# Kernel tuning notes

Hardware: AMD Instinct MI355X
Metric: run time of the kernel (lower is better)

The kernel has to match this reference:

```python
import jax, jax.numpy as jnp
import numpy as np

B, P, E, H = 2, 4096, 512, 8
D = E // H
EPS = 1e-5


def _layernorm2d(x, g, b):
    # LayerNorm over last two dims (patches, embed) jointly, per torch nn.LayerNorm([P, E])
    mu = jnp.mean(x, axis=(-2, -1), keepdims=True)
    var = jnp.mean(jnp.square(x - mu), axis=(-2, -1), keepdims=True)
    return (x - mu) * jax.lax.rsqrt(var + EPS) * g + b


def setup_inputs() -> dict:
    key = jax.random.key(0)
    ks = jax.random.split(key, 4)
    s_in = 1.0 / np.sqrt(E)
    s_hid = 1.0 / np.sqrt(3 * E)
    return {
        "x": jax.random.normal(ks[0], (B, P, E), dtype=jnp.float32),
        "g1": jnp.ones((P, E), jnp.float32),
        "b1": jnp.zeros((P, E), jnp.float32),
        "W1": jax.random.normal(ks[1], (3 * E, E), jnp.float32) * s_in,
        "g2": jnp.ones((P, E), jnp.float32),
        "b2": jnp.zeros((P, E), jnp.float32),
        "Wa": jax.random.normal(ks[2], (3 * E, E), jnp.float32) * s_in,
        "ba": jnp.zeros((3 * E,), jnp.float32),
        "Wb": jax.random.normal(ks[3], (E, 3 * E), jnp.float32) * s_hid,
        "bb": jnp.zeros((E,), jnp.float32),
    }


def reference(x, g1, b1, W1, g2, b2, Wa, ba, Wb, bb):
    # --- attention branch ---
    h = _layernorm2d(x, g1, b1)                      # [B,P,E]
    qkv = h @ W1.T                                   # [B,P,3E]
    qkv = qkv.reshape(B, P, 3, H, D).transpose(2, 0, 3, 1, 4)  # [3,B,H,P,D]
    q, k, v = qkv[0], qkv[1], qkv[2]
    scale = 1.0 / jnp.sqrt(jnp.float32(D))
    dp = jnp.einsum("bhqd,bhkd->bhqk", q, k) * scale  # [B,H,P,P]
    # NOTE: softmax over axis -2 (the query axis), as in the original code
    dp = jax.nn.softmax(dp, axis=-2)
    wv = jnp.einsum("bhqk,bhkd->bhqd", dp, v)        # [B,H,P,D]
    wv = wv.transpose(0, 2, 1, 3).reshape(B, P, E)   # [B,P,E]
    out1 = x + wv
    # --- MLP branch ---
    h2 = _layernorm2d(out1, g2, b2)
    h2 = jax.nn.gelu(h2 @ Wa.T + ba, approximate=False)
    h2 = jax.nn.gelu(h2 @ Wb.T + bb, approximate=False)
    return h2 + out1
```

## Files before the change

### kernel.cpp

```cpp
#include <hip/hip_runtime.h>
#include <math.h>

typedef __bf16 bf16x8 __attribute__((ext_vector_type(8)));
typedef float f32x4 __attribute__((ext_vector_type(4)));
typedef unsigned short u16;
typedef unsigned int u32;

__device__ __forceinline__ void gl_lds16(const void* g, void* l) {
  __builtin_amdgcn_global_load_lds(
      (const __attribute__((address_space(1))) void*)g,
      (__attribute__((address_space(3))) void*)l, 16, 0, 0);
}

__device__ __forceinline__ u16 f2bf(float x) {
  union { float f; u32 u; } v; v.f = x;
  u32 r = v.u + 0x7FFFu + ((v.u >> 16) & 1u);
  return (u16)(r >> 16);
}

__device__ __forceinline__ float gelu_f(float v) {
  return 0.5f * v * (1.0f + erff(v * 0.7071067811865475f));
}

__global__ void castbf(const float* __restrict__ s, u16* __restrict__ d) {
  int i = blockIdx.x * 256 + threadIdx.x;
  float4 v = ((const float4*)s)[i];
  uint2 o;
  o.x = (u32)f2bf(v.x) | ((u32)f2bf(v.y) << 16);
  o.y = (u32)f2bf(v.z) | ((u32)f2bf(v.w) << 16);
  ((uint2*)d)[i] = o;
}

__global__ void ln_reduce(const float* __restrict__ src, float2* __restrict__ part) {
  int b = blockIdx.y;
  const float4* p = (const float4*)(src + (size_t)b * 2097152 + (size_t)blockIdx.x * 16384);
  float s = 0.f, q = 0.f;
  #pragma unroll
  for (int i = 0; i < 16; i++) {
    float4 v = p[i * 256 + threadIdx.x];
    s += v.x + v.y + v.z + v.w;
    q += v.x * v.x + v.y * v.y + v.z * v.z + v.w * v.w;
  }
  #pragma unroll
  for (int off = 32; off; off >>= 1) { s += __shfl_down(s, off, 64); q += __shfl_down(q, off, 64); }
  __shared__ float ls[4], lq[4];
  int w = threadIdx.x >> 6;
  if ((threadIdx.x & 63) == 0) { ls[w] = s; lq[w] = q; }
  __syncthreads();
  if (threadIdx.x == 0)
    part[b * 128 + blockIdx.x] =
        make_float2(ls[0] + ls[1] + ls[2] + ls[3], lq[0] + lq[1] + lq[2] + lq[3]);
}

__global__ void ln_final(const float2* __restrict__ part, float2* __restrict__ stats) {
  int b = blockIdx.x, t = threadIdx.x;
  float2 a = part[b * 128 + t], c = part[b * 128 + 64 + t];
  float s = a.x + c.x, q = a.y + c.y;
  #pragma unroll
  for (int off = 32; off; off >>= 1) { s += __shfl_down(s, off, 64); q += __shfl_down(q, off, 64); }
  if (t == 0) {
    const float inv = 1.0f / 2097152.0f;
    float mu = s * inv, var = q * inv - mu * mu;
    stats[b] = make_float2(mu, rsqrtf(var + 1e-5f));
  }
}

__global__ void ln_apply(const float* __restrict__ src, const float* __restrict__ g,
                         const float* __restrict__ bta, const float2* __restrict__ stats,
                         u16* __restrict__ dst) {
  int i = blockIdx.x * 256 + threadIdx.x;
  int b = i >= 524288;
  float2 st = stats[b];
  int r = i - b * 524288;
  float4 v = ((const float4*)src)[i];
  float4 gv = ((const float4*)g)[r];
  float4 bv = ((const float4*)bta)[r];
  float h0 = (v.x - st.x) * st.y * gv.x + bv.x;
  float h1 = (v.y - st.x) * st.y * gv.y + bv.y;
  float h2 = (v.z - st.x) * st.y * gv.z + bv.z;
  float h3 = (v.w - st.x) * st.y * gv.w + bv.w;
  uint2 o;
  o.x = (u32)f2bf(h0) | ((u32)f2bf(h1) << 16);
  o.y = (u32)f2bf(h2) | ((u32)f2bf(h3) << 16);
  ((uint2*)dst)[i] = o;
}

template <int MODE>
__global__ __launch_bounds__(256, 2)
void gemm_bt(const u16* __restrict__ A, const u16* __restrict__ Bm,
             const float* __restrict__ bias, const float* __restrict__ res,
             float* __restrict__ outf, u16* __restrict__ outb,
             int M, int N, int K) {
  __shared__ u16 As[128 * 32], Bs[128 * 32];
  const int tid = threadIdx.x;
  const int m0 = blockIdx.y * 128, n0 = blockIdx.x * 128;
  const int lane = tid & 63, w = tid >> 6;
  const int wm = (w >> 1) * 64, wn = (w & 1) * 64;
  const int c = lane & 15, quad = lane >> 4;
  const int arow = tid >> 2, acol = (tid & 3) * 8;

  const u16* gA = A + (size_t)(m0 + arow) * K + acol;
  const u16* gB = Bm + (size_t)(n0 + arow) * K + acol;
  u16* lA = As + tid * 8;
  u16* lB = Bs + tid * 8;

  f32x4 acc[4][4] = {};
  for (int kt = 0; kt < K; kt += 32) {
    gl_lds16(gA, lA);
    gl_lds16(gA + (size_t)64 * K, lA + 64 * 32);
    gl_lds16(gB, lB);
    gl_lds16(gB + (size_t)64 * K, lB + 64 * 32);
    gA += 32; gB += 32;
    __syncthreads();
    bf16x8 af[4], bf[4];
    #pragma unroll
    for (int i = 0; i < 4; i++) {
      af[i] = *(const bf16x8*)&As[(wm + i * 16 + c) * 32 + quad * 8];
      bf[i] = *(const bf16x8*)&Bs[(wn + i * 16 + c) * 32 + quad * 8];
    }
    #pragma unroll
    for (int i = 0; i < 4; i++)
      #pragma unroll
      for (int j = 0; j < 4; j++)
        acc[i][j] = __builtin_amdgcn_mfma_f32_16x16x32_bf16(af[i], bf[j], acc[i][j], 0, 0, 0);
    __syncthreads();
  }
  #pragma unroll
  for (int i = 0; i < 4; i++) {
    const int row0 = m0 + wm + i * 16 + quad * 4;
    #pragma unroll
    for (int j = 0; j < 4; j++) {
      const int col = n0 + wn + j * 16 + c;
      #pragma unroll
      for (int r = 0; r < 4; r++) {
        float v = acc[i][j][r];
        size_t oi = (size_t)(row0 + r) * N + col;
        if (MODE == 1 || MODE == 2) v = gelu_f(v + bias[col]);
        if (MODE == 2) outf[oi] = v + res[oi];
        else           outb[oi] = f2bf(v);
      }
    }
  }
}

__global__ void vtrans(const u16* __restrict__ qkv, u16* __restrict__ vt) {
  __shared__ u16 t[64 * 66];
  int bh = blockIdx.y, p0 = blockIdx.x * 64;
  int b = bh >> 3, h = bh & 7;
  const u16* src = qkv + ((size_t)(b * 4096 + p0)) * 1536 + 1024 + h * 64;
  int tid = threadIdx.x;
  #pragma unroll
  for (int j = 0; j < 16; j++) {
    int idx = j * 256 + tid;
    int p = idx >> 6, d = idx & 63;
    t[d * 66 + p] = src[(size_t)p * 1536 + d];
  }
  __syncthreads();
  u16* dst = vt + (size_t)bh * 64 * 4096 + p0;
  #pragma unroll
  for (int j = 0; j < 16; j++) {
    int idx = j * 256 + tid;
    int d = idx >> 6, p = idx & 63;
    dst[(size_t)d * 4096 + p] = t[d * 66 + p];
  }
}

__global__ __launch_bounds__(256, 2)
void attn_pass1(const u16* __restrict__ qkv, float* __restrict__ rl) {
  __shared__ u16 Ks[2 * 128 * 32], Qs[2 * 128 * 32];
  __shared__ float colsum[128];
  const int tid = threadIdx.x;
  const int bh = blockIdx.y, b = bh >> 3, h = bh & 7;
  const int k0 = blockIdx.x * 128;
  const int lane = tid & 63, w = tid >> 6;
  const int wm = (w >> 1) * 64, wn = (w & 1) * 64;
  const int c = lane & 15, quad = lane >> 4;
  const int arow = tid >> 2, acol = (tid & 3) * 8;
  const u16* Kg = qkv + ((size_t)(b * 4096 + k0)) * 1536 + 512 + h * 64;
  const u16* Qg = qkv + ((size_t)(b * 4096)) * 1536 + h * 64;

  #pragma unroll
  for (int ks = 0; ks < 2; ks++)
    #pragma unroll
    for (int rr = 0; rr < 128; rr += 64)
      gl_lds16(Kg + (size_t)(rr + arow) * 1536 + ks * 32 + acol,
               Ks + ks * 4096 + (rr + arow) * 32 + acol);
  if (tid < 128) colsum[tid] = 0.f;

  float sacc[4] = {0.f, 0.f, 0.f, 0.f};
  for (int qt = 0; qt < 32; qt++) {
    #pragma unroll
    for (int ks = 0; ks < 2; ks++)
      #pragma unroll
      for (int rr = 0; rr < 128; rr += 64)
        gl_lds16(Qg + (size_t)(qt * 128 + rr + arow) * 1536 + ks * 32 + acol,
                 Qs + ks * 4096 + (rr + arow) * 32 + acol);
    __syncthreads();
    f32x4 acc[4][4] = {};
    #pragma unroll
    for (int ks = 0; ks < 2; ks++) {
      bf16x8 af[4], bf[4];
      #pragma unroll
      for (int i = 0; i < 4; i++) {
        af[i] = *(const bf16x8*)&Qs[ks * 4096 + (wm + i * 16 + c) * 32 + quad * 8];
        bf[i] = *(const bf16x8*)&Ks[ks * 4096 + (wn + i * 16 + c) * 32 + quad * 8];
      }
      #pragma unroll
      for (int i = 0; i < 4; i++)
        #pragma unroll
        for (int j = 0; j < 4; j++)
          acc[i][j] = __builtin_amdgcn_mfma_f32_16x16x32_bf16(af[i], bf[j], acc[i][j], 0, 0, 0);
    }
    #pragma unroll
    for (int j = 0; j < 4; j++) {
      float t = 0.f;
      #pragma unroll
      for (int i = 0; i < 4; i++)
        #pragma unroll
        for (int r = 0; r < 4; r++)
          t += __expf(acc[i][j][r] * 0.125f);
      sacc[j] += t;
    }
    __syncthreads();
  }
  #pragma unroll
  for (int j = 0; j < 4; j++) {
    float v = sacc[j];
    v += __shfl_xor(v, 16, 64);
    v += __shfl_xor(v, 32, 64);
    if (quad == 0) atomicAdd(&colsum[wn + j * 16 + c], v);
  }
  __syncthreads();
  if (tid < 128) rl[(size_t)bh * 4096 + k0 + tid] = 1.0f / colsum[tid];
}

__global__ __launch_bounds__(256, 2)
void attn_pass2(const u16* __restrict__ qkv, const u16* __restrict__ vt,
                const float* __restrict__ rl, const float* __restrict__ x,
                float* __restrict__ out1) {
  __shared__ u16 Qs[2 * 128 * 32];
  __shared__ u16 Ks[2 * 128 * 32];
  __shared__ u16 Vs[4 * 64 * 32];
  __shared__ u16 Ps[4 * 128 * 32];
  const int tid = threadIdx.x;
  const int bh = blockIdx.y, b = bh >> 3, h = bh & 7;
  const int q0 = blockIdx.x * 128;
  const int lane = tid & 63, w = tid >> 6;
  const int wm = (w >> 1) * 64, wn = (w & 1) * 64;
  const int wn2 = (w & 1) * 32;
  const int c = lane & 15, quad = lane >> 4;
  const int arow = tid >> 2, acol = (tid & 3) * 8;
  const u16* Qg = qkv + ((size_t)(b * 4096 + q0)) * 1536 + h * 64;
  const u16* Kg = qkv + ((size_t)(b * 4096)) * 1536 + 512 + h * 64;
  const u16* Vg = vt + (size_t)bh * 64 * 4096;
  const float* rlg = rl + (size_t)bh * 4096;

  #pragma unroll
  for (int ks = 0; ks < 2; ks++)
    #pragma unroll
    for (int rr = 0; rr < 128; rr += 64)
      gl_lds16(Qg + (size_t)(rr + arow) * 1536 + ks * 32 + acol,
               Qs + ks * 4096 + (rr + arow) * 32 + acol);

  f32x4 oacc[4][2] = {};
  for (int kt = 0; kt < 32; kt++) {
    const int k0 = kt * 128;
    #pragma unroll
    for (int ks = 0; ks < 2; ks++)
      #pragma unroll
      for (int rr = 0; rr < 128; rr += 64)
        gl_lds16(Kg + (size_t)(k0 + rr + arow) * 1536 + ks * 32 + acol,
                 Ks + ks * 4096 + (rr + arow) * 32 + acol);
    #pragma unroll
    for (int kp = 0; kp < 4; kp++)
      gl_lds16(Vg + (size_t)arow * 4096 + k0 + kp * 32 + acol,
               Vs + kp * 2048 + arow * 32 + acol);
    __syncthreads();
    f32x4 sacc[4][4] = {};
    #pragma unroll
    for (int ks = 0; ks < 2; ks++) {
      bf16x8 af[4], bf[4];
      #pragma unroll
      for (int i = 0; i < 4; i++) {
        af[i] = *(const bf16x8*)&Qs[ks * 4096 + (wm + i * 16 + c) * 32 + quad * 8];
        bf[i] = *(const bf16x8*)&Ks[ks * 4096 + (wn + i * 16 + c) * 32 + quad * 8];
      }
      #pragma unroll
      for (int i = 0; i < 4; i++)
        #pragma unroll
        for (int j = 0; j < 4; j++)
          sacc[i][j] = __builtin_amdgcn_mfma_f32_16x16x32_bf16(af[i], bf[j], sacc[i][j], 0, 0, 0);
    }
    float rlv[4];
    #pragma unroll
    for (int j = 0; j < 4; j++) rlv[j] = rlg[k0 + wn + j * 16 + c];
    #pragma unroll
    for (int i = 0; i < 4; i++)
      #pragma unroll
      for (int j = 0; j < 4; j++) {
        const int kk = wn + j * 16 + c;
        u16* pp = Ps + (kk >> 5) * 4096 + (kk & 31);
        #pragma unroll
        for (int r = 0; r < 4; r++) {
          const int qq = wm + i * 16 + quad * 4 + r;
          pp[qq * 32] = f2bf(__expf(sacc[i][j][r] * 0.125f) * rlv[j]);
        }
      }
    __syncthreads();
    #pragma unroll
    for (int ks = 0; ks < 4; ks++) {
      bf16x8 pf[4], vf[2];
      #pragma unroll
      for (int i = 0; i < 4; i++)
        pf[i] = *(const bf16x8*)&Ps[ks * 4096 + (wm + i * 16 + c) * 32 + quad * 8];
      #pragma unroll
      for (int j = 0; j < 2; j++)
        vf[j] = *(const bf16x8*)&Vs[ks * 2048 + (wn2 + j * 16 + c) * 32 + quad * 8];
      #pragma unroll
      for (int i = 0; i < 4; i++)
        #pragma unroll
        for (int j = 0; j < 2; j++)
          oacc[i][j] = __builtin_amdgcn_mfma_f32_16x16x32_bf16(pf[i], vf[j], oacc[i][j], 0, 0, 0);
    }
    __syncthreads();
  }
  #pragma unroll
  for (int i = 0; i < 4; i++)
    #pragma unroll
    for (int j = 0; j < 2; j++)
      #pragma unroll
      for (int r = 0; r < 4; r++) {
        const int qq = q0 + wm + i * 16 + quad * 4 + r;
        const int dd = wn2 + j * 16 + c;
        size_t oi = ((size_t)(b * 4096 + qq)) * 512 + h * 64 + dd;
        out1[oi] = x[oi] + oacc[i][j][r];
      }
}

extern "C" void kernel_launch(void* const* d_in, const int* in_sizes, int n_in,
                              void* d_out, int out_size, void* d_ws, size_t ws_size,
                              hipStream_t stream) {
  const float* x  = (const float*)d_in[0];
  const float* g1 = (const float*)d_in[1];
  const float* b1 = (const float*)d_in[2];
  const float* W1 = (const float*)d_in[3];
  const float* g2 = (const float*)d_in[4];
  const float* b2 = (const float*)d_in[5];
  const float* Wa = (const float*)d_in[6];
  const float* ba = (const float*)d_in[7];
  const float* Wb = (const float*)d_in[8];
  const float* bb = (const float*)d_in[9];
  float* out = (float*)d_out;

  char* ws = (char*)d_ws;
  u16* w1b   = (u16*)(ws);
  u16* wab   = (u16*)(ws + 1572864);
  u16* wbb   = (u16*)(ws + 3145728);
  u16* h1    = (u16*)(ws + 4718592);
  u16* qkv   = (u16*)(ws + 13107200);
  u16* vt    = (u16*)(ws + 38273024);
  u16* h2    = (u16*)(ws + 46661632);
  u16* mid   = (u16*)(ws + 55050240);
  float* rl  = (float*)(ws + 80216064);
  float* o1  = (float*)(ws + 80478208);
  float2* part  = (float2*)(ws + 97255424);
  float2* stats = (float2*)(ws + 97257472);

  castbf<<<768, 256, 0, stream>>>(W1, w1b);
  castbf<<<768, 256, 0, stream>>>(Wa, wab);
  castbf<<<768, 256, 0, stream>>>(Wb, wbb);

  ln_reduce<<<dim3(128, 2), 256, 0, stream>>>(x, part);
  ln_final<<<2, 64, 0, stream>>>(part, stats);
  ln_apply<<<4096, 256, 0, stream>>>(x, g1, b1, stats, h1);

  gemm_bt<0><<<dim3(12, 64), 256, 0, stream>>>(h1, w1b, nullptr, nullptr, nullptr, qkv,
                                               8192, 1536, 512);
  vtrans<<<dim3(64, 16), 256, 0, stream>>>(qkv, vt);
  attn_pass1<<<dim3(32, 16), 256, 0, stream>>>(qkv, rl);
  attn_pass2<<<dim3(32, 16), 256, 0, stream>>>(qkv, vt, rl, x, o1);

  ln_reduce<<<dim3(128, 2), 256, 0, stream>>>(o1, part);
  ln_final<<<2, 64, 0, stream>>>(part, stats);
  ln_apply<<<4096, 256, 0, stream>>>(o1, g2, b2, stats, h2);

  gemm_bt<1><<<dim3(12, 64), 256, 0, stream>>>(h2, wab, ba, nullptr, nullptr, mid,
                                               8192, 1536, 512);
  gemm_bt<2><<<dim3(4, 64), 256, 0, stream>>>(mid, wbb, bb, o1, out, nullptr,
                                              8192, 512, 1536);
}
```

Before: 417.7 us.

## Fold column-softmax normalization into V and restructure attention passes around register-held Q/K

Pre-scales Q by 1/sqrt(D) in the QKV GEMM epilogue and folds the per-key reciprocal column sum into V during the transpose, so pass2 no longer reads rl or multiplies per element. Pass1 is rewritten to keep each wave's K fragments in registers and stream Q straight from global memory, with no LDS or block syncs. Pass2 keeps Q fragments in registers, computes transposed score tiles, writes packed bf16 P into a swizzled LDS layout, and drops one barrier per iteration. The three weight casts are merged into one launch. Costs include an extra rounding of V and Q to bf16 and global-latency exposure in pass1.

Result: slower. 454.1 us (+8.7%).

```diff
diff --git a/kernel.cpp b/kernel.cpp
--- a/kernel.cpp
+++ b/kernel.cpp
@@ -18,12 +18,24 @@
   return (u16)(r >> 16);
 }
 
+__device__ __forceinline__ u32 pack_bf2(float a, float b) {
+  union { float f; u32 u; } ua, ub; ua.f = a; ub.f = b;
+  return ((ua.u + 0x8000u) >> 16) | ((ub.u + 0x8000u) & 0xFFFF0000u);
+}
+
 __device__ __forceinline__ float gelu_f(float v) {
   return 0.5f * v * (1.0f + erff(v * 0.7071067811865475f));
 }
 
-__global__ void castbf(const float* __restrict__ s, u16* __restrict__ d) {
-  int i = blockIdx.x * 256 + threadIdx.x;
+__global__ void castbf3(const float* __restrict__ s0, const float* __restrict__ s1,
+                        const float* __restrict__ s2, u16* __restrict__ d0,
+                        u16* __restrict__ d1, u16* __restrict__ d2) {
+  int blk = blockIdx.x;
+  const float* s; u16* d;
+  if (blk < 768)       { s = s0; d = d0; }
+  else if (blk < 1536) { s = s1; d = d1; blk -= 768; }
+  else                 { s = s2; d = d2; blk -= 1536; }
+  int i = blk * 256 + threadIdx.x;
   float4 v = ((const float4*)s)[i];
   uint2 o;
   o.x = (u32)f2bf(v.x) | ((u32)f2bf(v.y) << 16);
@@ -135,6 +147,7 @@
       for (int r = 0; r < 4; r++) {
         float v = acc[i][j][r];
         size_t oi = (size_t)(row0 + r) * N + col;
+        if (MODE == 0 && col < 512) v *= 0.125f;
         if (MODE == 1 || MODE == 2) v = gelu_f(v + bias[col]);
         if (MODE == 2) outf[oi] = v + res[oi];
         else           outb[oi] = f2bf(v);
@@ -143,17 +156,71 @@
   }
 }
 
-__global__ void vtrans(const u16* __restrict__ qkv, u16* __restrict__ vt) {
+__global__ __launch_bounds__(256, 2)
+void attn_pass1(const u16* __restrict__ qkv, float* __restrict__ rl) {
+  const int tid = threadIdx.x;
+  const int bh = blockIdx.y, b = bh >> 3, h = bh & 7;
+  const int k0 = blockIdx.x * 128;
+  const int lane = tid & 63, w = tid >> 6;
+  const int wn = w * 32;
+  const int c = lane & 15, quad = lane >> 4;
+
+  bf16x8 bk[2][2];
+  {
+    const u16* Kg = qkv + ((size_t)(b * 4096 + k0 + wn + c)) * 1536 + 512 + h * 64 + quad * 8;
+    #pragma unroll
+    for (int j = 0; j < 2; j++)
+      #pragma unroll
+      for (int ks = 0; ks < 2; ks++)
+        bk[j][ks] = *(const bf16x8*)(Kg + (size_t)j * 16 * 1536 + ks * 32);
+  }
+  const u16* Qg = qkv + ((size_t)(b * 4096 + c)) * 1536 + h * 64 + quad * 8;
+
+  float s0 = 0.f, s1 = 0.f;
+  for (int qt = 0; qt < 64; qt++) {
+    f32x4 acc[4][2] = {};
+    #pragma unroll
+    for (int i4 = 0; i4 < 4; i4++) {
+      const u16* qp = Qg + (size_t)(qt * 64 + i4 * 16) * 1536;
+      bf16x8 a0 = *(const bf16x8*)(qp);
+      bf16x8 a1 = *(const bf16x8*)(qp + 32);
+      acc[i4][0] = __builtin_amdgcn_mfma_f32_16x16x32_bf16(a0, bk[0][0], acc[i4][0], 0, 0, 0);
+      acc[i4][0] = __builtin_amdgcn_mfma_f32_16x16x32_bf16(a1, bk[0][1], acc[i4][0], 0, 0, 0);
+      acc[i4][1] = __builtin_amdgcn_mfma_f32_16x16x32_bf16(a0, bk[1][0], acc[i4][1], 0, 0, 0);
+      acc[i4][1] = __builtin_amdgcn_mfma_f32_16x16x32_bf16(a1, bk[1][1], acc[i4][1], 0, 0, 0);
+    }
+    #pragma unroll
+    for (int i4 = 0; i4 < 4; i4++) {
+      #pragma unroll
+      for (int r = 0; r < 4; r++) {
+        s0 += __expf(acc[i4][0][r]);
+        s1 += __expf(acc[i4][1][r]);
+      }
+    }
+  }
+  s0 += __shfl_xor(s0, 16, 64); s0 += __shfl_xor(s0, 32, 64);
+  s1 += __shfl_xor(s1, 16, 64); s1 += __shfl_xor(s1, 32, 64);
+  if (quad == 0) {
+    rl[(size_t)bh * 4096 + k0 + wn + c]      = 1.0f / s0;
+    rl[(size_t)bh * 4096 + k0 + wn + 16 + c] = 1.0f / s1;
+  }
+}
+
+__global__ void vtrans(const u16* __restrict__ qkv, const float* __restrict__ rl,
+                       u16* __restrict__ vt) {
   __shared__ u16 t[64 * 66];
   int bh = blockIdx.y, p0 = blockIdx.x * 64;
   int b = bh >> 3, h = bh & 7;
   const u16* src = qkv + ((size_t)(b * 4096 + p0)) * 1536 + 1024 + h * 64;
+  const float* rp = rl + (size_t)bh * 4096 + p0;
   int tid = threadIdx.x;
   #pragma unroll
   for (int j = 0; j < 16; j++) {
     int idx = j * 256 + tid;
     int p = idx >> 6, d = idx & 63;
-    t[d * 66 + p] = src[(size_t)p * 1536 + d];
+    union { float f; u32 u; } uv;
+    uv.u = ((u32)src[(size_t)p * 1536 + d]) << 16;
+    t[d * 66 + p] = f2bf(uv.f * rp[p]);
   }
   __syncthreads();
   u16* dst = vt + (size_t)bh * 64 * 4096 + p0;
@@ -166,79 +233,8 @@
 }
 
 __global__ __launch_bounds__(256, 2)
-void attn_pass1(const u16* __restrict__ qkv, float* __restrict__ rl) {
-  __shared__ u16 Ks[2 * 128 * 32], Qs[2 * 128 * 32];
-  __shared__ float colsum[128];
-  const int tid = threadIdx.x;
-  const int bh = blockIdx.y, b = bh >> 3, h = bh & 7;
-  const int k0 = blockIdx.x * 128;
-  const int lane = tid & 63, w = tid >> 6;
-  const int wm = (w >> 1) * 64, wn = (w & 1) * 64;
-  const int c = lane & 15, quad = lane >> 4;
-  const int arow = tid >> 2, acol = (tid & 3) * 8;
-  const u16* Kg = qkv + ((size_t)(b * 4096 + k0)) * 1536 + 512 + h * 64;
-  const u16* Qg = qkv + ((size_t)(b * 4096)) * 1536 + h * 64;
-
-  #pragma unroll
-  for (int ks = 0; ks < 2; ks++)
-    #pragma unroll
-    for (int rr = 0; rr < 128; rr += 64)
-      gl_lds16(Kg + (size_t)(rr + arow) * 1536 + ks * 32 + acol,
-               Ks + ks * 4096 + (rr + arow) * 32 + acol);
-  if (tid < 128) colsum[tid] = 0.f;
-
-  float sacc[4] = {0.f, 0.f, 0.f, 0.f};
-  for (int qt = 0; qt < 32; qt++) {
-    #pragma unroll
-    for (int ks = 0; ks < 2; ks++)
-      #pragma unroll
-      for (int rr = 0; rr < 128; rr += 64)
-        gl_lds16(Qg + (size_t)(qt * 128 + rr + arow) * 1536 + ks * 32 + acol,
-                 Qs + ks * 4096 + (rr + arow) * 32 + acol);
-    __syncthreads();
-    f32x4 acc[4][4] = {};
-    #pragma unroll
-    for (int ks = 0; ks < 2; ks++) {
-      bf16x8 af[4], bf[4];
-      #pragma unroll
-      for (int i = 0; i < 4; i++) {
-        af[i] = *(const bf16x8*)&Qs[ks * 4096 + (wm + i * 16 + c) * 32 + quad * 8];
-        bf[i] = *(const bf16x8*)&Ks[ks * 4096 + (wn + i * 16 + c) * 32 + quad * 8];
-      }
-      #pragma unroll
-      for (int i = 0; i < 4; i++)
-        #pragma unroll
-        for (int j = 0; j < 4; j++)
-          acc[i][j] = __builtin_amdgcn_mfma_f32_16x16x32_bf16(af[i], bf[j], acc[i][j], 0, 0, 0);
-    }
-    #pragma unroll
-    for (int j = 0; j < 4; j++) {
-      float t = 0.f;
-      #pragma unroll
-      for (int i = 0; i < 4; i++)
-        #pragma unroll
-        for (int r = 0; r < 4; r++)
-          t += __expf(acc[i][j][r] * 0.125f);
-      sacc[j] += t;
-    }
-    __syncthreads();
-  }
-  #pragma unroll
-  for (int j = 0; j < 4; j++) {
-    float v = sacc[j];
-    v += __shfl_xor(v, 16, 64);
-    v += __shfl_xor(v, 32, 64);
-    if (quad == 0) atomicAdd(&colsum[wn + j * 16 + c], v);
-  }
-  __syncthreads();
-  if (tid < 128) rl[(size_t)bh * 4096 + k0 + tid] = 1.0f / colsum[tid];
-}
-
-__global__ __launch_bounds__(256, 2)
 void attn_pass2(const u16* __restrict__ qkv, const u16* __restrict__ vt,
-                const float* __restrict__ rl, const float* __restrict__ x,
-                float* __restrict__ out1) {
-  __shared__ u16 Qs[2 * 128 * 32];
+                const float* __restrict__ x, float* __restrict__ out1) {
   __shared__ u16 Ks[2 * 128 * 32];
   __shared__ u16 Vs[4 * 64 * 32];
   __shared__ u16 Ps[4 * 128 * 32];
@@ -246,23 +242,23 @@
   const int bh = blockIdx.y, b = bh >> 3, h = bh & 7;
   const int q0 = blockIdx.x * 128;
   const int lane = tid & 63, w = tid >> 6;
-  const int wm = (w >> 1) * 64, wn = (w & 1) * 64;
-  const int wn2 = (w & 1) * 32;
+  const int wq = w * 32;
   const int c = lane & 15, quad = lane >> 4;
   const int arow = tid >> 2, acol = (tid & 3) * 8;
-  const u16* Qg = qkv + ((size_t)(b * 4096 + q0)) * 1536 + h * 64;
+
+  bf16x8 bq[2][2];
+  {
+    const u16* Qg = qkv + ((size_t)(b * 4096 + q0 + wq + c)) * 1536 + h * 64 + quad * 8;
+    #pragma unroll
+    for (int j = 0; j < 2; j++)
+      #pragma unroll
+      for (int ks = 0; ks < 2; ks++)
+        bq[j][ks] = *(const bf16x8*)(Qg + (size_t)j * 16 * 1536 + ks * 32);
+  }
   const u16* Kg = qkv + ((size_t)(b * 4096)) * 1536 + 512 + h * 64;
   const u16* Vg = vt + (size_t)bh * 64 * 4096;
-  const float* rlg = rl + (size_t)bh * 4096;
-
-  #pragma unroll
-  for (int ks = 0; ks < 2; ks++)
-    #pragma unroll
-    for (int rr = 0; rr < 128; rr += 64)
-      gl_lds16(Qg + (size_t)(rr + arow) * 1536 + ks * 32 + acol,
-               Qs + ks * 4096 + (rr + arow) * 32 + acol);
-
-  f32x4 oacc[4][2] = {};
+
+  f32x4 oacc[2][4] = {};
   for (int kt = 0; kt < 32; kt++) {
     const int k0 = kt * 128;
     #pragma unroll
@@ -276,64 +272,69 @@
       gl_lds16(Vg + (size_t)arow * 4096 + k0 + kp * 32 + acol,
                Vs + kp * 2048 + arow * 32 + acol);
     __syncthreads();
-    f32x4 sacc[4][4] = {};
-    #pragma unroll
-    for (int ks = 0; ks < 2; ks++) {
-      bf16x8 af[4], bf[4];
-      #pragma unroll
-      for (int i = 0; i < 4; i++) {
-        af[i] = *(const bf16x8*)&Qs[ks * 4096 + (wm + i * 16 + c) * 32 + quad * 8];
-        bf[i] = *(const bf16x8*)&Ks[ks * 4096 + (wn + i * 16 + c) * 32 + quad * 8];
-      }
-      #pragma unroll
-      for (int i = 0; i < 4; i++)
+
+    #pragma unroll
+    for (int ih = 0; ih < 2; ih++) {
+      f32x4 sacc[4][2] = {};
+      #pragma unroll
+      for (int i4 = 0; i4 < 4; i4++) {
+        const int i = ih * 4 + i4;
+        bf16x8 af0 = *(const bf16x8*)&Ks[(i * 16 + c) * 32 + quad * 8];
+        bf16x8 af1 = *(const bf16x8*)&Ks[4096 + (i * 16 + c) * 32 + quad * 8];
+        sacc[i4][0] = __builtin_amdgcn_mfma_f32_16x16x32_bf16(af0, bq[0][0], sacc[i4][0], 0, 0, 0);
+        sacc[i4][0] = __builtin_amdgcn_mfma_f32_16x16x32_bf16(af1, bq[0][1], sacc[i4][0], 0, 0, 0);
+        sacc[i4][1] = __builtin_amdgcn_mfma_f32_16x16x32_bf16(af0, bq[1][0], sacc[i4][1], 0, 0, 0);
+        sacc[i4][1] = __builtin_amdgcn_mfma_f32_16x16x32_bf16(af1, bq[1][1], sacc[i4][1], 0, 0, 0);
+      }
+      #pragma unroll
+      for (int i4 = 0; i4 < 4; i4++) {
+        const int i = ih * 4 + i4;
         #pragma unroll
-        for (int j = 0; j < 4; j++)
-          sacc[i][j] = __builtin_amdgcn_mfma_f32_16x16x32_bf16(af[i], bf[j], sacc[i][j], 0, 0, 0);
-    }
-    float rlv[4];
-    #pragma unroll
-    for (int j = 0; j < 4; j++) rlv[j] = rlg[k0 + wn + j * 16 + c];
-    #pragma unroll
-    for (int i = 0; i < 4; i++)
-      #pragma unroll
-      for (int j = 0; j < 4; j++) {
-        const int kk = wn + j * 16 + c;
-        u16* pp = Ps + (kk >> 5) * 4096 + (kk & 31);
+        for (int j = 0; j < 2; j++) {
+          const int qloc = wq + j * 16 + c;
+          const int sl = ((i & 1) * 4 + quad) ^ (((qloc >> 1) & 3) << 1);
+          u16* pp = Ps + (i >> 1) * 4096 + qloc * 32 + sl * 4;
+          float e0 = __expf(sacc[i4][j][0]);
+          float e1 = __expf(sacc[i4][j][1]);
+          float e2 = __expf(sacc[i4][j][2]);
+          float e3 = __expf(sacc[i4][j][3]);
+          uint2 pk;
+          pk.x = pack_bf2(e0, e1);
+          pk.y = pack_bf2(e2, e3);
+          *(uint2*)pp = pk;
+        }
+      }
+    }
+    #pragma unroll
+    for (int ksb = 0; ksb < 4; ksb++) {
+      bf16x8 pf[2], vf[4];
+      #pragma unroll
+      for (int i2 = 0; i2 < 2; i2++) {
+        const int qloc = wq + i2 * 16 + c;
+        const int blk = quad ^ ((qloc >> 1) & 3);
+        pf[i2] = *(const bf16x8*)&Ps[ksb * 4096 + qloc * 32 + blk * 8];
+      }
+      #pragma unroll
+      for (int j2 = 0; j2 < 4; j2++)
+        vf[j2] = *(const bf16x8*)&Vs[ksb * 2048 + (j2 * 16 + c) * 32 + quad * 8];
+      #pragma unroll
+      for (int i2 = 0; i2 < 2; i2++)
         #pragma unroll
-        for (int r = 0; r < 4; r++) {
-          const int qq = wm + i * 16 + quad * 4 + r;
-          pp[qq * 32] = f2bf(__expf(sacc[i][j][r] * 0.125f) * rlv[j]);
-        }
-      }
+        for (int j2 = 0; j2 < 4; j2++)
+          oacc[i2][j2] = __builtin_amdgcn_mfma_f32_16x16x32_bf16(pf[i2], vf[j2], oacc[i2][j2], 0, 0, 0);
+    }
     __syncthreads();
-    #pragma unroll
-    for (int ks = 0; ks < 4; ks++) {
-      bf16x8 pf[4], vf[2];
-      #pragma unroll
-      for (int i = 0; i < 4; i++)
-        pf[i] = *(const bf16x8*)&Ps[ks * 4096 + (wm + i * 16 + c) * 32 + quad * 8];
-      #pragma unroll
-      for (int j = 0; j < 2; j++)
-        vf[j] = *(const bf16x8*)&Vs[ks * 2048 + (wn2 + j * 16 + c) * 32 + quad * 8];
-      #pragma unroll
-      for (int i = 0; i < 4; i++)
-        #pragma unroll
-        for (int j = 0; j < 2; j++)
-          oacc[i][j] = __builtin_amdgcn_mfma_f32_16x16x32_bf16(pf[i], vf[j], oacc[i][j], 0, 0, 0);
-    }
-    __syncthreads();
-  }
-  #pragma unroll
-  for (int i = 0; i < 4; i++)
-    #pragma unroll
-    for (int j = 0; j < 2; j++)
+  }
+  #pragma unroll
+  for (int i2 = 0; i2 < 2; i2++)
+    #pragma unroll
+    for (int j2 = 0; j2 < 4; j2++)
       #pragma unroll
       for (int r = 0; r < 4; r++) {
-        const int qq = q0 + wm + i * 16 + quad * 4 + r;
-        const int dd = wn2 + j * 16 + c;
-        size_t oi = ((size_t)(b * 4096 + qq)) * 512 + h * 64 + dd;
-        out1[oi] = x[oi] + oacc[i][j][r];
+        const int q = q0 + wq + i2 * 16 + quad * 4 + r;
+        const int d = j2 * 16 + c;
+        size_t oi = ((size_t)(b * 4096 + q)) * 512 + h * 64 + d;
+        out1[oi] = x[oi] + oacc[i2][j2][r];
       }
 }
 
@@ -366,9 +367,7 @@
   float2* part  = (float2*)(ws + 97255424);
   float2* stats = (float2*)(ws + 97257472);
 
-  castbf<<<768, 256, 0, stream>>>(W1, w1b);
-  castbf<<<768, 256, 0, stream>>>(Wa, wab);
-  castbf<<<768, 256, 0, stream>>>(Wb, wbb);
+  castbf3<<<2304, 256, 0, stream>>>(W1, Wa, Wb, w1b, wab, wbb);
 
   ln_reduce<<<dim3(128, 2), 256, 0, stream>>>(x, part);
   ln_final<<<2, 64, 0, stream>>>(part, stats);
@@ -376,9 +375,9 @@
 
   gemm_bt<0><<<dim3(12, 64), 256, 0, stream>>>(h1, w1b, nullptr, nullptr, nullptr, qkv,
                                                8192, 1536, 512);
-  vtrans<<<dim3(64, 16), 256, 0, stream>>>(qkv, vt);
   attn_pass1<<<dim3(32, 16), 256, 0, stream>>>(qkv, rl);
-  attn_pass2<<<dim3(32, 16), 256, 0, stream>>>(qkv, vt, rl, x, o1);
+  vtrans<<<dim3(64, 16), 256, 0, stream>>>(qkv, rl, vt);
+  attn_pass2<<<dim3(32, 16), 256, 0, stream>>>(qkv, vt, x, o1);
 
   ln_reduce<<<dim3(128, 2), 256, 0, stream>>>(o1, part);
   ln_final<<<2, 64, 0, stream>>>(part, stats);
```
